# Optimization experiments

Measured on AMD Instinct MI355X. Metric: run time of the kernel, lower is better.

The kernel has to match this reference:

```python
import jax, jax.numpy as jnp
import numpy as np

B, L, D, DEG = 32, 1024, 512, 8
E = B * L * DEG  # 262144 edges total
N = B * L


def setup_inputs() -> dict:
    key = jax.random.key(0)
    ks = jax.random.split(key, 8)
    text_feature = jax.random.normal(ks[0], (B, L, D), jnp.float32)
    # edge list per sample (torch.nonzero(edge_matrix[i]) equivalent), offset by b*L like PyG batching
    src_local = jax.random.randint(ks[1], (E,), 0, L, jnp.int32)
    dst_local = jax.random.randint(ks[2], (E,), 0, L, jnp.int32)
    boff = (jnp.arange(E, dtype=jnp.int32) // (E // B)) * L
    edge_src = src_local + boff
    edge_dst = dst_local + boff
    s = 1.0 / np.sqrt(D)
    W1 = jax.random.uniform(ks[3], (D, D), jnp.float32, -s, s)   # node Linear
    b1 = jax.random.uniform(ks[4], (D,), jnp.float32, -s, s)
    gamma = jnp.ones((D,), jnp.float32)      # BatchNorm1d weight
    beta = jnp.zeros((D,), jnp.float32)      # BatchNorm1d bias
    run_mean = jnp.zeros((D,), jnp.float32)  # BN running stats (eval mode)
    run_var = jnp.ones((D,), jnp.float32)
    alpha1 = jnp.array(0.25, jnp.float32)    # PReLU (node MLP)
    Wg = jax.random.uniform(ks[5], (D, D), jnp.float32, -s, s)   # GCNConv lin (bias=False)
    bg = jnp.zeros((D,), jnp.float32)        # GCNConv bias
    alpha2 = jnp.array(0.25, jnp.float32)    # PReLU (after GCN)
    return {"text_feature": text_feature, "edge_src": edge_src, "edge_dst": edge_dst,
            "W1": W1, "b1": b1, "gamma": gamma, "beta": beta,
            "run_mean": run_mean, "run_var": run_var, "alpha1": alpha1,
            "Wg": Wg, "bg": bg, "alpha2": alpha2}


def reference(text_feature, edge_src, edge_dst, W1, b1, gamma, beta,
              run_mean, run_var, alpha1, Wg, bg, alpha2):
    Bs, Ls, Ds = text_feature.shape
    Nn = Bs * Ls
    xf = text_feature.reshape(Nn, Ds)
    # node MLP: Linear -> BatchNorm1d (eval) -> PReLU
    h = xf @ W1 + b1
    h = (h - run_mean) * jax.lax.rsqrt(run_var + 1e-5) * gamma + beta
    h = jnp.where(h >= 0, h, alpha1 * h)
    # GCNConv: add self loops, symmetric degree norm, gather->scatter-add, + bias
    nodes = jnp.arange(Nn, dtype=edge_src.dtype)
    src = jnp.concatenate([edge_src, nodes])
    dst = jnp.concatenate([edge_dst, nodes])
    deg = jnp.zeros((Nn,), h.dtype).at[dst].add(1.0)  # in-degree incl. self loop, >= 1
    dinv = jax.lax.rsqrt(deg)
    xw = h @ Wg                               # [N, D]
    msg = (xw * dinv[:, None])[src]           # gather D^{-1/2}-scaled messages [E+N, D]
    agg = jnp.zeros_like(xw).at[dst].add(msg) * dinv[:, None]
    g = agg + bg
    g = jnp.where(g >= 0, g, alpha2 * g)      # PReLU
    g = g.reshape(Bs, Ls, Ds)
    # F.normalize(p=2, dim=2) + residual (original input)
    g = g / jnp.clip(jnp.linalg.norm(g, axis=2, keepdims=True), 1e-12)
    return g + text_feature
```

## Files before the change

### kernel.cpp

```cpp
#include <hip/hip_runtime.h>
#include <math.h>

#define DD    512
#define NN    32768
#define EE    262144

typedef float f32x4 __attribute__((ext_vector_type(4)));
typedef __bf16 bf16x8 __attribute__((ext_vector_type(8)));

#define AS1 __attribute__((address_space(1)))
#define AS3 __attribute__((address_space(3)))

__global__ void k_zero(int* __restrict__ cnt) {
    int i = blockIdx.x * 256 + threadIdx.x;
    if (i < NN) cnt[i] = 0;
}

__global__ void k_count(const int* __restrict__ dst, int* __restrict__ cnt) {
    int e = blockIdx.x * 256 + threadIdx.x;
    if (e < EE) atomicAdd(&cnt[dst[e]], 1);
}

__global__ __launch_bounds__(1024) void k_scan(
    const int* __restrict__ cnt, int* __restrict__ offs,
    int* __restrict__ cursor, float* __restrict__ dinv)
{
    __shared__ int part[1024];
    int t = threadIdx.x;
    int base = t * 32;
    int local[32];
    int s = 0;
#pragma unroll
    for (int i = 0; i < 32; ++i) { local[i] = s; s += cnt[base + i]; }
    part[t] = s;
    __syncthreads();
    for (int off = 1; off < 1024; off <<= 1) {
        int v = (t >= off) ? part[t - off] : 0;
        __syncthreads();
        part[t] += v;
        __syncthreads();
    }
    int prev = (t == 0) ? 0 : part[t - 1];
#pragma unroll
    for (int i = 0; i < 32; ++i) {
        int o = prev + local[i];
        offs[base + i] = o;
        cursor[base + i] = o;
        dinv[base + i] = rsqrtf((float)cnt[base + i] + 1.0f);
    }
    if (t == 1023) offs[NN] = part[1023];
}

__global__ void k_fill(const int* __restrict__ src, const int* __restrict__ dst,
                       int* __restrict__ cursor, int* __restrict__ csr) {
    int e = blockIdx.x * 256 + threadIdx.x;
    if (e < EE) {
        int d = dst[e];
        int p = atomicAdd(&cursor[d], 1);
        csr[p] = src[e];
    }
}

__global__ __launch_bounds__(256) void k_wt(const float* __restrict__ W1, const float* __restrict__ Wg,
                                            __bf16* __restrict__ W1t, __bf16* __restrict__ Wgt) {
    __shared__ float tile[32][33];
    const float* W = blockIdx.z ? Wg : W1;
    __bf16* Wt = blockIdx.z ? Wgt : W1t;
    int x0 = blockIdx.x * 32;
    int y0 = blockIdx.y * 32;
    int tx = threadIdx.x;
    for (int j = threadIdx.y; j < 32; j += 8)
        tile[j][tx] = W[(size_t)(y0 + j) * DD + x0 + tx];
    __syncthreads();
    for (int j = threadIdx.y; j < 32; j += 8)
        Wt[(size_t)(x0 + j) * DD + y0 + tx] = (__bf16)tile[tx][j];
}

template <int MODE>
__global__ __launch_bounds__(256, 2) void k_gemm_w(
    const void* __restrict__ Ap,
    const __bf16* __restrict__ Wt,
    __bf16* __restrict__ Cout,
    const float* __restrict__ bias,
    const float* __restrict__ gamma, const float* __restrict__ beta,
    const float* __restrict__ mean, const float* __restrict__ var,
    const float* __restrict__ alphap)
{
    __shared__ __bf16 slab[2][16384];

    const int t    = threadIdx.x;
    const int lane = t & 63;
    const int wv   = t >> 6;
    const int work = ((blockIdx.x & 7) << 6) + (blockIdx.x >> 3);
    const int mbase   = (work >> 2) * 256;
    const int colbase = (work & 3) * 128 + wv * 32;

    bf16x8 wf[2][16];
#pragma unroll
    for (int C = 0; C < 2; ++C)
#pragma unroll
        for (int kf = 0; kf < 16; ++kf) {
            int col = colbase + C * 16 + (lane & 15);
            wf[C][kf] = *(const bf16x8*)(Wt + (size_t)col * DD + kf * 32 + (lane >> 4) * 8);
        }

    float s0 = 0, s1 = 0, t0 = 0, t1 = 0, al = 0;
    if constexpr (MODE == 1) {
        int c0 = colbase + (lane & 15), c1 = c0 + 16;
        float r0 = rsqrtf(var[c0] + 1e-5f), r1 = rsqrtf(var[c1] + 1e-5f);
        s0 = gamma[c0] * r0;  s1 = gamma[c1] * r1;
        t0 = (bias[c0] - mean[c0]) * s0 + beta[c0];
        t1 = (bias[c1] - mean[c1]) * s1 + beta[c1];
        al = alphap[0];
    }

    auto stage2 = [&](int bb, int mt) {
        const __bf16* A = (const __bf16*)Ap;
#pragma unroll
        for (int i = 0; i < 8; ++i) {
            int d  = i * 256 + wv * 64 + lane;
            int kf = d >> 7, r = (d >> 2) & 31, s = d & 3;
            int c  = kf * 4 + (s ^ ((r >> 1) & 3));
            const __bf16* g = A + (size_t)(mbase + mt * 32 + r) * DD + c * 8;
            __builtin_amdgcn_global_load_lds(
                (const AS1 unsigned int*)g,
                (AS3 unsigned int*)(&slab[bb][(size_t)(i * 256 + wv * 64) * 8]), 16, 0, 0);
        }
    };

    float4 fa[4][2];
    auto loadh = [&](int h, int mt) {
        const float* A = (const float*)Ap;
#pragma unroll
        for (int q = 0; q < 4; ++q) {
            int d  = (h * 4 + q) * 256 + t;
            int kf = d >> 7, r = (d >> 2) & 31, s = d & 3;
            int c  = kf * 4 + (s ^ ((r >> 1) & 3));
            const float* g = A + (size_t)(mbase + mt * 32 + r) * DD + c * 8;
            fa[q][0] = *(const float4*)g;
            fa[q][1] = *(const float4*)(g + 4);
        }
    };
    auto writeh = [&](int h, int bb) {
#pragma unroll
        for (int q = 0; q < 4; ++q) {
            int d = (h * 4 + q) * 256 + t;
            bf16x8 o;
            o[0] = (__bf16)fa[q][0].x; o[1] = (__bf16)fa[q][0].y;
            o[2] = (__bf16)fa[q][0].z; o[3] = (__bf16)fa[q][0].w;
            o[4] = (__bf16)fa[q][1].x; o[5] = (__bf16)fa[q][1].y;
            o[6] = (__bf16)fa[q][1].z; o[7] = (__bf16)fa[q][1].w;
            *(bf16x8*)&slab[bb][(size_t)d * 8] = o;
        }
    };

    if constexpr (MODE == 1) {
        loadh(0, 0); writeh(0, 0);
        loadh(1, 0); writeh(1, 0);
        asm volatile("s_waitcnt lgkmcnt(0)" ::: "memory");
    } else {
        stage2(0, 0);
        asm volatile("s_waitcnt vmcnt(0)" ::: "memory");
    }
    __builtin_amdgcn_s_barrier();

    for (int mt = 0; mt < 8; ++mt) {
        const int cur = mt & 1, nxt = cur ^ 1;
        const __bf16* sl = &slab[cur][0];

        if (mt < 7) {
            if constexpr (MODE == 1) loadh(0, mt + 1);
            else                     stage2(nxt, mt + 1);
        }
        asm volatile("" ::: "memory");

        f32x4 acc[2][2] = {};
        auto rdA = [&](int kf, int half) -> bf16x8 {
            int r = half * 16 + (lane & 15);
            int s = (lane >> 4) ^ ((r >> 1) & 3);
            return *(const bf16x8*)&sl[kf * 1024 + r * 32 + s * 8];
        };
        bf16x8 a0c = rdA(0, 0), a1c = rdA(0, 1), a0n, a1n;
#pragma unroll
        for (int kf = 0; kf < 16; ++kf) {
            if (kf < 15) { a0n = rdA(kf + 1, 0); a1n = rdA(kf + 1, 1); }
            acc[0][0] = __builtin_amdgcn_mfma_f32_16x16x32_bf16(a0c, wf[0][kf], acc[0][0], 0, 0, 0);
            acc[0][1] = __builtin_amdgcn_mfma_f32_16x16x32_bf16(a0c, wf[1][kf], acc[0][1], 0, 0, 0);
            acc[1][0] = __builtin_amdgcn_mfma_f32_16x16x32_bf16(a1c, wf[0][kf], acc[1][0], 0, 0, 0);
            acc[1][1] = __builtin_amdgcn_mfma_f32_16x16x32_bf16(a1c, wf[1][kf], acc[1][1], 0, 0, 0);
            if constexpr (MODE == 1) {
                if (kf == 7 && mt < 7) {
                    writeh(0, nxt);
                    loadh(1, mt + 1);
                }
            }
            a0c = a0n; a1c = a1n;
        }
        if constexpr (MODE == 1) {
            if (mt < 7) writeh(1, nxt);
        } else {
            if (mt < 7) asm volatile("s_waitcnt vmcnt(0)" ::: "memory");
        }

#pragma unroll
        for (int R = 0; R < 2; ++R)
#pragma unroll
            for (int C = 0; C < 2; ++C) {
                int col  = colbase + C * 16 + (lane & 15);
                int rowb = mbase + mt * 32 + R * 16 + ((lane >> 4) << 2);
                float ss = C ? s1 : s0, tt = C ? t1 : t0;
#pragma unroll
                for (int j = 0; j < 4; ++j) {
                    float x = acc[R][C][j];
                    if constexpr (MODE == 1) {
                        x = x * ss + tt;
                        x = (x >= 0.0f) ? x : al * x;
                    }
                    Cout[(size_t)(rowb + j) * DD + col] = (__bf16)x;
                }
            }

        if constexpr (MODE == 1) asm volatile("s_waitcnt lgkmcnt(0)" ::: "memory");
        asm volatile("" ::: "memory");
        __builtin_amdgcn_s_barrier();
    }
}

__global__ __launch_bounds__(256) void k_gather_final(
    const int* __restrict__ offs, const int* __restrict__ csr,
    const __bf16* __restrict__ xws, const float* __restrict__ dinv,
    const float* __restrict__ bg, const float* __restrict__ alpha2,
    const float* __restrict__ text, float* __restrict__ out)
{
    int blk = blockIdx.x;
    int sb  = ((blk & 7) << 10) + (blk >> 3);
    int wave = threadIdx.x >> 6;
    int lane = threadIdx.x & 63;
    int node = sb * 4 + wave;
    int c = lane * 8;
    int beg = offs[node], end = offs[node + 1];
    int ne = end - beg;

    float dn = dinv[node];
    bf16x8 sv = *(const bf16x8*)(xws + (size_t)node * DD + c);
    float a[8];
#pragma unroll
    for (int i = 0; i < 8; ++i) a[i] = dn * (float)sv[i];

    int k = 0;
    for (; k + 4 <= ne; k += 4) {
        int s0 = csr[beg + k + 0];
        int s1 = csr[beg + k + 1];
        int s2 = csr[beg + k + 2];
        int s3 = csr[beg + k + 3];
        float d0 = dinv[s0], d1 = dinv[s1], d2 = dinv[s2], d3 = dinv[s3];
        bf16x8 v0 = *(const bf16x8*)(xws + (size_t)s0 * DD + c);
        bf16x8 v1 = *(const bf16x8*)(xws + (size_t)s1 * DD + c);
        bf16x8 v2 = *(const bf16x8*)(xws + (size_t)s2 * DD + c);
        bf16x8 v3 = *(const bf16x8*)(xws + (size_t)s3 * DD + c);
#pragma unroll
        for (int i = 0; i < 8; ++i)
            a[i] += d0 * (float)v0[i] + d1 * (float)v1[i] + d2 * (float)v2[i] + d3 * (float)v3[i];
    }
    for (; k < ne; ++k) {
        int s = csr[beg + k];
        float ds_ = dinv[s];
        bf16x8 v = *(const bf16x8*)(xws + (size_t)s * DD + c);
#pragma unroll
        for (int i = 0; i < 8; ++i) a[i] += ds_ * (float)v[i];
    }

    float al = alpha2[0];
    float g[8];
    float ss = 0.0f;
#pragma unroll
    for (int i = 0; i < 8; ++i) {
        float x = a[i] * dn + bg[c + i];
        x = (x >= 0.0f) ? x : al * x;
        g[i] = x;
        ss += x * x;
    }
#pragma unroll
    for (int off = 1; off < 64; off <<= 1) ss += __shfl_xor(ss, off, 64);
    float inv = 1.0f / fmaxf(sqrtf(ss), 1e-12f);

    float4 t0 = *(const float4*)(text + (size_t)node * DD + c);
    float4 t1 = *(const float4*)(text + (size_t)node * DD + c + 4);
    float4 o0, o1;
    o0.x = g[0] * inv + t0.x; o0.y = g[1] * inv + t0.y;
    o0.z = g[2] * inv + t0.z; o0.w = g[3] * inv + t0.w;
    o1.x = g[4] * inv + t1.x; o1.y = g[5] * inv + t1.y;
    o1.z = g[6] * inv + t1.z; o1.w = g[7] * inv + t1.w;
    *(float4*)(out + (size_t)node * DD + c)     = o0;
    *(float4*)(out + (size_t)node * DD + c + 4) = o1;
}

extern "C" void kernel_launch(void* const* d_in, const int* in_sizes, int n_in,
                              void* d_out, int out_size, void* d_ws, size_t ws_size,
                              hipStream_t stream) {
    const float* text   = (const float*)d_in[0];
    const int*   esrc   = (const int*)d_in[1];
    const int*   edst   = (const int*)d_in[2];
    const float* W1     = (const float*)d_in[3];
    const float* b1     = (const float*)d_in[4];
    const float* gamma  = (const float*)d_in[5];
    const float* beta   = (const float*)d_in[6];
    const float* rmean  = (const float*)d_in[7];
    const float* rvar   = (const float*)d_in[8];
    const float* alpha1 = (const float*)d_in[9];
    const float* Wg     = (const float*)d_in[10];
    const float* bg     = (const float*)d_in[11];
    const float* alpha2 = (const float*)d_in[12];
    float* out = (float*)d_out;

    char* p = (char*)d_ws;
    auto alloc = [&](size_t bytes) { char* r = p; p += (bytes + 255) & ~(size_t)255; return r; };
    int*    cnt     = (int*)alloc((size_t)NN * 4);
    int*    offs    = (int*)alloc((size_t)(NN + 1) * 4);
    int*    cursor  = (int*)alloc((size_t)NN * 4);
    float*  dinv    = (float*)alloc((size_t)NN * 4);
    int*    csr     = (int*)alloc((size_t)EE * 4);
    __bf16* W1t     = (__bf16*)alloc((size_t)DD * DD * 2);
    __bf16* Wgt     = (__bf16*)alloc((size_t)DD * DD * 2);
    __bf16* h_bf    = (__bf16*)alloc((size_t)NN * DD * 2);
    __bf16* xws     = (__bf16*)alloc((size_t)NN * DD * 2);

    k_zero<<<NN / 256, 256, 0, stream>>>(cnt);
    k_count<<<EE / 256, 256, 0, stream>>>(edst, cnt);
    k_scan<<<1, 1024, 0, stream>>>(cnt, offs, cursor, dinv);
    k_fill<<<EE / 256, 256, 0, stream>>>(esrc, edst, cursor, csr);

    k_wt<<<dim3(16, 16, 2), dim3(32, 8), 0, stream>>>(W1, Wg, W1t, Wgt);

    k_gemm_w<1><<<512, 256, 0, stream>>>(text, W1t, h_bf, b1, gamma, beta, rmean, rvar, alpha1);

    k_gemm_w<2><<<512, 256, 0, stream>>>(h_bf, Wgt, xws, nullptr, nullptr, nullptr, nullptr, nullptr, nullptr);

    k_gather_final<<<NN / 4, 256, 0, stream>>>(offs, csr, xws, dinv, bg, alpha2, text, out);
}
```

Measured before the change: 142.8 us.

## Replace weight-stationary GEMM with 256x256 tiled LDS double-buffered GEMM

Result: slower. 167.2 us (+17.1%).

```diff
diff --git a/kernel.cpp b/kernel.cpp
--- a/kernel.cpp
+++ b/kernel.cpp
@@ -77,7 +77,7 @@
 }
 
 template <int MODE>
-__global__ __launch_bounds__(256, 2) void k_gemm_w(
+__global__ __launch_bounds__(512, 2) void k_gemm_256(
     const void* __restrict__ Ap,
     const __bf16* __restrict__ Wt,
     __bf16* __restrict__ Cout,
@@ -86,143 +86,144 @@
     const float* __restrict__ mean, const float* __restrict__ var,
     const float* __restrict__ alphap)
 {
-    __shared__ __bf16 slab[2][16384];
+    __shared__ __bf16 As[2][16384];
+    __shared__ __bf16 Bs[2][16384];
 
     const int t    = threadIdx.x;
     const int lane = t & 63;
     const int wv   = t >> 6;
-    const int work = ((blockIdx.x & 7) << 6) + (blockIdx.x >> 3);
-    const int mbase   = (work >> 2) * 256;
-    const int colbase = (work & 3) * 128 + wv * 32;
-
-    bf16x8 wf[2][16];
-#pragma unroll
-    for (int C = 0; C < 2; ++C)
-#pragma unroll
-        for (int kf = 0; kf < 16; ++kf) {
-            int col = colbase + C * 16 + (lane & 15);
-            wf[C][kf] = *(const bf16x8*)(Wt + (size_t)col * DD + kf * 32 + (lane >> 4) * 8);
-        }
-
-    float s0 = 0, s1 = 0, t0 = 0, t1 = 0, al = 0;
-    if constexpr (MODE == 1) {
-        int c0 = colbase + (lane & 15), c1 = c0 + 16;
-        float r0 = rsqrtf(var[c0] + 1e-5f), r1 = rsqrtf(var[c1] + 1e-5f);
-        s0 = gamma[c0] * r0;  s1 = gamma[c1] * r1;
-        t0 = (bias[c0] - mean[c0]) * s0 + beta[c0];
-        t1 = (bias[c1] - mean[c1]) * s1 + beta[c1];
-        al = alphap[0];
-    }
-
-    auto stage2 = [&](int bb, int mt) {
-        const __bf16* A = (const __bf16*)Ap;
-#pragma unroll
-        for (int i = 0; i < 8; ++i) {
-            int d  = i * 256 + wv * 64 + lane;
-            int kf = d >> 7, r = (d >> 2) & 31, s = d & 3;
-            int c  = kf * 4 + (s ^ ((r >> 1) & 3));
-            const __bf16* g = A + (size_t)(mbase + mt * 32 + r) * DD + c * 8;
+    const int l15  = lane & 15;
+    const int lhi  = lane >> 4;
+    const int work = ((blockIdx.x & 7) << 5) + (blockIdx.x >> 3);
+    const int m0   = (work >> 1) * 256;
+    const int n0   = (work & 1) * 256;
+    const int wm   = (wv >> 2) * 128;
+    const int wn   = (wv & 3) * 64;
+
+    auto stageB = [&](int bb, int k0) {
+#pragma unroll
+        for (int i = 0; i < 4; ++i) {
+            int d = i * 512 + wv * 64 + lane;
+            int c = d & 255, gs = d >> 8;
+            const __bf16* g = Wt + (size_t)(n0 + c) * DD + k0 + (gs >> 2) * 32 + (gs & 3) * 8;
             __builtin_amdgcn_global_load_lds(
                 (const AS1 unsigned int*)g,
-                (AS3 unsigned int*)(&slab[bb][(size_t)(i * 256 + wv * 64) * 8]), 16, 0, 0);
+                (AS3 unsigned int*)(&Bs[bb][(i * 512 + wv * 64) * 8]), 16, 0, 0);
         }
     };
-
-    float4 fa[4][2];
-    auto loadh = [&](int h, int mt) {
+    auto stageA2 = [&](int bb, int k0) {
+        const __bf16* A = (const __bf16*)Ap;
+#pragma unroll
+        for (int i = 0; i < 4; ++i) {
+            int d = i * 512 + wv * 64 + lane;
+            int r = d & 255, gs = d >> 8;
+            const __bf16* g = A + (size_t)(m0 + r) * DD + k0 + (gs >> 2) * 32 + (gs & 3) * 8;
+            __builtin_amdgcn_global_load_lds(
+                (const AS1 unsigned int*)g,
+                (AS3 unsigned int*)(&As[bb][(i * 512 + wv * 64) * 8]), 16, 0, 0);
+        }
+    };
+    float4 fa[2][2];
+    auto loadAh = [&](int h, int k0) {
         const float* A = (const float*)Ap;
 #pragma unroll
-        for (int q = 0; q < 4; ++q) {
-            int d  = (h * 4 + q) * 256 + t;
-            int kf = d >> 7, r = (d >> 2) & 31, s = d & 3;
-            int c  = kf * 4 + (s ^ ((r >> 1) & 3));
-            const float* g = A + (size_t)(mbase + mt * 32 + r) * DD + c * 8;
+        for (int q = 0; q < 2; ++q) {
+            int d = (h * 2 + q) * 512 + t;
+            int r = d & 255, gs = d >> 8;
+            const float* g = A + (size_t)(m0 + r) * DD + k0 + (gs >> 2) * 32 + (gs & 3) * 8;
             fa[q][0] = *(const float4*)g;
             fa[q][1] = *(const float4*)(g + 4);
         }
     };
-    auto writeh = [&](int h, int bb) {
-#pragma unroll
-        for (int q = 0; q < 4; ++q) {
-            int d = (h * 4 + q) * 256 + t;
+    auto writeAh = [&](int h, int bb) {
+#pragma unroll
+        for (int q = 0; q < 2; ++q) {
+            int d = (h * 2 + q) * 512 + t;
             bf16x8 o;
             o[0] = (__bf16)fa[q][0].x; o[1] = (__bf16)fa[q][0].y;
             o[2] = (__bf16)fa[q][0].z; o[3] = (__bf16)fa[q][0].w;
             o[4] = (__bf16)fa[q][1].x; o[5] = (__bf16)fa[q][1].y;
             o[6] = (__bf16)fa[q][1].z; o[7] = (__bf16)fa[q][1].w;
-            *(bf16x8*)&slab[bb][(size_t)d * 8] = o;
+            *(bf16x8*)&As[bb][(size_t)d * 8] = o;
         }
     };
 
     if constexpr (MODE == 1) {
-        loadh(0, 0); writeh(0, 0);
-        loadh(1, 0); writeh(1, 0);
-        asm volatile("s_waitcnt lgkmcnt(0)" ::: "memory");
+        loadAh(0, 0); writeAh(0, 0);
+        loadAh(1, 0); writeAh(1, 0);
+        stageB(0, 0);
+        asm volatile("s_waitcnt vmcnt(0) lgkmcnt(0)" ::: "memory");
     } else {
-        stage2(0, 0);
-        asm volatile("s_waitcnt vmcnt(0)" ::: "memory");
-    }
-    __builtin_amdgcn_s_barrier();
-
-    for (int mt = 0; mt < 8; ++mt) {
-        const int cur = mt & 1, nxt = cur ^ 1;
-        const __bf16* sl = &slab[cur][0];
-
-        if (mt < 7) {
-            if constexpr (MODE == 1) loadh(0, mt + 1);
-            else                     stage2(nxt, mt + 1);
-        }
+        stageA2(0, 0); stageB(0, 0);
+    }
+
+    f32x4 acc[8][4] = {};
+
+#pragma unroll
+    for (int kt = 0; kt < 8; ++kt) {
+        const int cur = kt & 1, nxt = cur ^ 1;
+        const int k1 = (kt + 1) * 64;
+
+        if (kt < 7) {
+            if constexpr (MODE == 1) { loadAh(0, k1); stageB(nxt, k1); }
+            else                     { stageA2(nxt, k1); stageB(nxt, k1); }
+        }
+
+        if (kt < 7) asm volatile("s_waitcnt vmcnt(8)" ::: "memory");
+        else        asm volatile("s_waitcnt vmcnt(0)" ::: "memory");
+        __builtin_amdgcn_s_barrier();
         asm volatile("" ::: "memory");
 
-        f32x4 acc[2][2] = {};
-        auto rdA = [&](int kf, int half) -> bf16x8 {
-            int r = half * 16 + (lane & 15);
-            int s = (lane >> 4) ^ ((r >> 1) & 3);
-            return *(const bf16x8*)&sl[kf * 1024 + r * 32 + s * 8];
-        };
-        bf16x8 a0c = rdA(0, 0), a1c = rdA(0, 1), a0n, a1n;
-#pragma unroll
-        for (int kf = 0; kf < 16; ++kf) {
-            if (kf < 15) { a0n = rdA(kf + 1, 0); a1n = rdA(kf + 1, 1); }
-            acc[0][0] = __builtin_amdgcn_mfma_f32_16x16x32_bf16(a0c, wf[0][kf], acc[0][0], 0, 0, 0);
-            acc[0][1] = __builtin_amdgcn_mfma_f32_16x16x32_bf16(a0c, wf[1][kf], acc[0][1], 0, 0, 0);
-            acc[1][0] = __builtin_amdgcn_mfma_f32_16x16x32_bf16(a1c, wf[0][kf], acc[1][0], 0, 0, 0);
-            acc[1][1] = __builtin_amdgcn_mfma_f32_16x16x32_bf16(a1c, wf[1][kf], acc[1][1], 0, 0, 0);
+#pragma unroll
+        for (int g = 0; g < 2; ++g) {
+            bf16x8 af[8], bfr[4];
+#pragma unroll
+            for (int m = 0; m < 8; ++m)
+                af[m] = *(const bf16x8*)&As[cur][((g * 4 + lhi) * 256 + wm + m * 16 + l15) * 8];
+#pragma unroll
+            for (int n = 0; n < 4; ++n)
+                bfr[n] = *(const bf16x8*)&Bs[cur][((g * 4 + lhi) * 256 + wn + n * 16 + l15) * 8];
+#pragma unroll
+            for (int m = 0; m < 8; ++m)
+#pragma unroll
+                for (int n = 0; n < 4; ++n)
+                    acc[m][n] = __builtin_amdgcn_mfma_f32_16x16x32_bf16(af[m], bfr[n], acc[m][n], 0, 0, 0);
             if constexpr (MODE == 1) {
-                if (kf == 7 && mt < 7) {
-                    writeh(0, nxt);
-                    loadh(1, mt + 1);
-                }
+                if (g == 0 && kt < 7) { writeAh(0, nxt); loadAh(1, k1); }
             }
-            a0c = a0n; a1c = a1n;
         }
         if constexpr (MODE == 1) {
-            if (mt < 7) writeh(1, nxt);
-        } else {
-            if (mt < 7) asm volatile("s_waitcnt vmcnt(0)" ::: "memory");
-        }
-
-#pragma unroll
-        for (int R = 0; R < 2; ++R)
-#pragma unroll
-            for (int C = 0; C < 2; ++C) {
-                int col  = colbase + C * 16 + (lane & 15);
-                int rowb = mbase + mt * 32 + R * 16 + ((lane >> 4) << 2);
-                float ss = C ? s1 : s0, tt = C ? t1 : t0;
-#pragma unroll
-                for (int j = 0; j < 4; ++j) {
-                    float x = acc[R][C][j];
-                    if constexpr (MODE == 1) {
-                        x = x * ss + tt;
-                        x = (x >= 0.0f) ? x : al * x;
-                    }
-                    Cout[(size_t)(rowb + j) * DD + col] = (__bf16)x;
-                }
-            }
-
-        if constexpr (MODE == 1) asm volatile("s_waitcnt lgkmcnt(0)" ::: "memory");
+            if (kt < 7) writeAh(1, nxt);
+            asm volatile("s_waitcnt lgkmcnt(0)" ::: "memory");
+        }
+
         asm volatile("" ::: "memory");
         __builtin_amdgcn_s_barrier();
+        asm volatile("" ::: "memory");
+    }
+
+#pragma unroll
+    for (int n = 0; n < 4; ++n) {
+        int col = n0 + wn + n * 16 + l15;
+        float sc = 1.0f, tc = 0.0f, al = 0.0f;
+        if constexpr (MODE == 1) {
+            sc = gamma[col] * rsqrtf(var[col] + 1e-5f);
+            tc = (bias[col] - mean[col]) * sc + beta[col];
+            al = alphap[0];
+        }
+#pragma unroll
+        for (int m = 0; m < 8; ++m) {
+            int rowb = m0 + wm + m * 16 + (lhi << 2);
+#pragma unroll
+            for (int j = 0; j < 4; ++j) {
+                float x = acc[m][n][j];
+                if constexpr (MODE == 1) {
+                    x = x * sc + tc;
+                    x = (x >= 0.0f) ? x : al * x;
+                }
+                Cout[(size_t)(rowb + j) * DD + col] = (__bf16)x;
+            }
+        }
     }
 }
 
@@ -284,15 +285,16 @@
     for (int off = 1; off < 64; off <<= 1) ss += __shfl_xor(ss, off, 64);
     float inv = 1.0f / fmaxf(sqrtf(ss), 1e-12f);
 
-    float4 t0 = *(const float4*)(text + (size_t)node * DD + c);
-    float4 t1 = *(const float4*)(text + (size_t)node * DD + c + 4);
+    size_t base = (size_t)node * DD + c;
+    float4 t0 = *(const float4*)&text[base];
+    float4 t1 = *(const float4*)&text[base + 4];
     float4 o0, o1;
     o0.x = g[0] * inv + t0.x; o0.y = g[1] * inv + t0.y;
     o0.z = g[2] * inv + t0.z; o0.w = g[3] * inv + t0.w;
     o1.x = g[4] * inv + t1.x; o1.y = g[5] * inv + t1.y;
     o1.z = g[6] * inv + t1.z; o1.w = g[7] * inv + t1.w;
-    *(float4*)(out + (size_t)node * DD + c)     = o0;
-    *(float4*)(out + (size_t)node * DD + c + 4) = o1;
+    *(float4*)&out[base]     = o0;
+    *(float4*)&out[base + 4] = o1;
 }
 
 extern "C" void kernel_launch(void* const* d_in, const int* in_sizes, int n_in,
@@ -332,9 +334,9 @@
 
     k_wt<<<dim3(16, 16, 2), dim3(32, 8), 0, stream>>>(W1, Wg, W1t, Wgt);
 
-    k_gemm_w<1><<<512, 256, 0, stream>>>(text, W1t, h_bf, b1, gamma, beta, rmean, rvar, alpha1);
-
-    k_gemm_w<2><<<512, 256, 0, stream>>>(h_bf, Wgt, xws, nullptr, nullptr, nullptr, nullptr, nullptr, nullptr);
+    k_gemm_256<1><<<256, 512, 0, stream>>>(text, W1t, h_bf, b1, gamma, beta, rmean, rvar, alpha1);
+
+    k_gemm_256<2><<<256, 512, 0, stream>>>(h_bf, Wgt, xws, nullptr, nullptr, nullptr, nullptr, nullptr, nullptr);
 
     k_gather_final<<<NN / 4, 256, 0, stream>>>(offs, csr, xws, dinv, bg, alpha2, text, out);
 }
```
